# Performance work log

Hardware: AMD Instinct MI355X
Metric: run time of the kernel (lower is better)

Reference implementation:

```python
import jax, jax.numpy as jnp
import numpy as np

N = 50000      # nodes
M = 800000     # edges
D = 128        # node_state_dim == msg_dim
EF = 32        # edge_feat_dim
DF = 32        # node_dist_feat_dim
ATT = 128      # att_hidden_dim
L = 2          # num_layer (num_prop = 1)
IN = D + EF + DF  # 192, MLP input dim


def setup_inputs() -> dict:
    key = jax.random.key(0)
    ks = jax.random.split(key, 18)
    rn = lambda k, shape, s=0.05: jax.random.normal(k, shape, dtype=jnp.float32) * s
    return {
        "node_feat":   rn(ks[0], (N, D), 1.0),
        "node_feat_c": rn(ks[1], (N, D), 1.0),
        "edge":        jax.random.randint(ks[2], (M, 2), 0, N, dtype=jnp.int32),
        "edge_feat":   rn(ks[3], (M, EF), 1.0),
        "dist_feat":   rn(ks[4], (M, DF), 1.0),
        # msg MLP: Linear(IN->D) -> ReLU -> Linear(D->D), stacked over layers
        "msg_w0": rn(ks[5], (L, IN, D)),  "msg_b0": jnp.zeros((L, D), jnp.float32),
        "msg_w1": rn(ks[6], (L, D, D)),   "msg_b1": jnp.zeros((L, D), jnp.float32),
        # attention head: Linear(IN->ATT) -> ReLU -> Linear(ATT->D) -> Sigmoid
        "att_w0": rn(ks[7], (L, IN, ATT)), "att_b0": jnp.zeros((L, ATT), jnp.float32),
        "att_w1": rn(ks[8], (L, ATT, D)),  "att_b1": jnp.zeros((L, D), jnp.float32),
        # LSTMCell params (torch layout: W_ih [4H, in], W_hh [4H, H], gate order i,f,g,o)
        "lstm_wih": rn(ks[9],  (L, 4 * D, D)),
        "lstm_whh": rn(ks[10], (L, 4 * D, D)),
        "lstm_bih": jnp.zeros((L, 4 * D), jnp.float32),
        "lstm_bhh": jnp.zeros((L, 4 * D), jnp.float32),
    }


def _lstm_cell(x, h, c, wih, whh, bih, bhh):
    gates = x @ wih.T + bih + h @ whh.T + bhh          # [N, 4D]
    i, f, g, o = jnp.split(gates, 4, axis=1)
    c2 = jax.nn.sigmoid(f) * c + jax.nn.sigmoid(i) * jnp.tanh(g)
    h2 = jax.nn.sigmoid(o) * jnp.tanh(c2)
    return h2, c2


def reference(node_feat, node_feat_c, edge, edge_feat, dist_feat,
              msg_w0, msg_b0, msg_w1, msg_b1,
              att_w0, att_b0, att_w1, att_b1,
              lstm_wih, lstm_whh, lstm_bih, lstm_bhh):
    src = edge[:, 0]
    dst = edge[:, 1]
    state, state_c = node_feat, node_feat_c
    for ii in range(L):
        if ii > 0:
            state = jax.nn.relu(state)
        # _prop (num_prop = 1)
        state_diff = state[src] - state[dst]                               # [M, D]
        edge_input = jnp.concatenate([state_diff, edge_feat, dist_feat], 1)  # [M, IN]
        msg = jax.nn.relu(edge_input @ msg_w0[ii] + msg_b0[ii]) @ msg_w1[ii] + msg_b1[ii]
        att = jax.nn.sigmoid(
            jax.nn.relu(edge_input @ att_w0[ii] + att_b0[ii]) @ att_w1[ii] + att_b1[ii])
        msg = msg * att
        state_msg = jax.ops.segment_sum(msg, dst, num_segments=N)          # scatter_add
        state, state_c = _lstm_cell(state_msg, state, state_c,
                                    lstm_wih[ii], lstm_whh[ii],
                                    lstm_bih[ii], lstm_bhh[ii])
    return state
```

## Files before the change

kernel.cpp:

```cpp
#include <hip/hip_runtime.h>

constexpr int N  = 50000;
constexpr int M  = 800000;
constexpr int D  = 128;
constexpr int IN = 192;
constexpr int TE = 64;

typedef __attribute__((ext_vector_type(4)))  short short4v;
typedef __attribute__((ext_vector_type(8)))  short short8;
typedef __attribute__((ext_vector_type(16))) float f32x16;

__device__ __align__(16) short g_wp[163840];
__device__ __align__(16) short g_lw[262144];
__device__ __align__(16) short g_efdf[(size_t)M * 64];
__device__ __align__(16) short g_sbf[(size_t)N * D];
__device__ int g_cnt[N];
__device__ int g_ssrc[M];
__device__ int g_sdst[M];
__device__ int g_pos[M];

__device__ __forceinline__ float sigm(float x) { return 1.0f / (1.0f + __expf(-x)); }

__device__ __forceinline__ short f2bf(float f) {
    unsigned u = __builtin_bit_cast(unsigned, f);
    u = (u + 0x7FFFu + ((u >> 16) & 1u)) >> 16;
    return (short)u;
}
__device__ __forceinline__ float bf2f(short s) {
    return __builtin_bit_cast(float, ((unsigned)(unsigned short)s) << 16);
}

__global__ void zero_cnt_kernel() {
    for (int i = blockIdx.x * 256 + threadIdx.x; i < N; i += gridDim.x * 256) g_cnt[i] = 0;
}
__global__ void hist_kernel(const int* __restrict__ edge) {
    int e = blockIdx.x * 256 + threadIdx.x;
    if (e < M) atomicAdd(&g_cnt[edge[e * 2 + 1]], 1);
}
__global__ void scan_kernel() {
    __shared__ int partial[256];
    const int t = threadIdx.x;
    const int CH = (N + 255) / 256;
    const int base = t * CH;
    int sum = 0;
    for (int i = 0; i < CH; ++i) { int idx = base + i; if (idx < N) sum += g_cnt[idx]; }
    partial[t] = sum;
    __syncthreads();
    if (t == 0) { int acc = 0; for (int i = 0; i < 256; ++i) { int x = partial[i]; partial[i] = acc; acc += x; } }
    __syncthreads();
    int run = partial[t];
    for (int i = 0; i < CH; ++i) {
        int idx = base + i;
        if (idx < N) { int c = g_cnt[idx]; g_cnt[idx] = run; run += c; }
    }
}
__global__ void scatter_kernel(const int* __restrict__ edge) {
    int e = blockIdx.x * 256 + threadIdx.x;
    if (e < M) {
        const int s = edge[e * 2], d = edge[e * 2 + 1];
        const int p = atomicAdd(&g_cnt[d], 1);
        g_pos[e]  = p;
        g_ssrc[p] = s;
        g_sdst[p] = d;
    }
}

__global__ void pack_edge(const float* __restrict__ w0m, const float* __restrict__ w0a,
                          const float* __restrict__ w1m, const float* __restrict__ w1a) {
    int gid = blockIdx.x * 256 + threadIdx.x;
    int ii = gid / 81920;
    int r  = gid % 81920;
    int p  = r / 40960;  r %= 40960;
    int which = (r >= 24576) ? 1 : 0;
    int r2 = which ? r - 24576 : r;
    int e    = r2 & 7;
    int f    = r2 >> 3;
    int lane = f & 63;
    int ktct = f >> 6;
    int ct = ktct & 3, kt = ktct >> 2;
    int k   = kt * 16 + ((lane >> 5) << 3) + e;
    int col = ct * 32 + (lane & 31);
    const float* w0 = p ? w0a : w0m;
    const float* w1 = p ? w1a : w1m;
    float v = which ? w1[((size_t)ii * D + k) * D + col]
                    : w0[((size_t)ii * IN + k) * D + col];
    g_wp[gid] = f2bf(v);
}

__global__ void pack_lstm(const float* __restrict__ wih, const float* __restrict__ whh) {
    int gid = blockIdx.x * 256 + threadIdx.x;
    int ii = gid >> 17;
    int r  = gid & 131071;
    int e = r & 7, f = r >> 3;
    int lane = f & 63, rest = f >> 6;
    int cf = rest & 15, kt = rest >> 4;
    int col = cf * 32 + (lane & 31);
    int k   = (kt & 7) * 16 + ((lane >> 5) << 3) + e;
    const float* src = (kt < 8) ? wih : whh;
    g_lw[gid] = f2bf(src[((size_t)ii * 512 + col) * D + k]);
}

__global__ void pack_efdf(const float* __restrict__ ef, const float* __restrict__ df) {
    int gid = blockIdx.x * 256 + threadIdx.x;
    int e = gid >> 3, c0 = (gid & 7) * 8;
    const float* s = (c0 < 32) ? (ef + (size_t)e * 32 + c0) : (df + (size_t)e * 32 + (c0 - 32));
    float4 u0 = *(const float4*)s, u1 = *(const float4*)(s + 4);
    short8 t;
    t[0] = f2bf(u0.x); t[1] = f2bf(u0.y); t[2] = f2bf(u0.z); t[3] = f2bf(u0.w);
    t[4] = f2bf(u1.x); t[5] = f2bf(u1.y); t[6] = f2bf(u1.z); t[7] = f2bf(u1.w);
    const size_t pos = (size_t)g_pos[e];
    *(short8*)(g_efdf + pos * 64 + (size_t)(gid & 7) * 8) = t;
}

__global__ void init_kernel(const float4* __restrict__ nf, const float4* __restrict__ nfc,
                            float4* __restrict__ state, float4* __restrict__ state_c) {
    const int total = N * D / 4;
    for (int i = blockIdx.x * blockDim.x + threadIdx.x; i < total; i += gridDim.x * blockDim.x) {
        state[i]   = nf[i];
        state_c[i] = nfc[i];
    }
}

__global__ void prep_kernel(float4* __restrict__ state, float4* __restrict__ msg, int do_relu) {
    const int total = N * D / 4;
    const float4 z = make_float4(0.f, 0.f, 0.f, 0.f);
    for (int i = blockIdx.x * blockDim.x + threadIdx.x; i < total; i += gridDim.x * blockDim.x) {
        float4 v = state[i];
        if (do_relu) {
            v.x = fmaxf(v.x, 0.f); v.y = fmaxf(v.y, 0.f);
            v.z = fmaxf(v.z, 0.f); v.w = fmaxf(v.w, 0.f);
            state[i] = v;
        }
        short4v b;
        b[0] = f2bf(v.x); b[1] = f2bf(v.y); b[2] = f2bf(v.z); b[3] = f2bf(v.w);
        *(short4v*)(g_sbf + (size_t)i * 4) = b;
        msg[i] = z;
    }
}

__device__ __forceinline__ void stage_ld(const short8* __restrict__ gsrc, int gc, short8 g[4], int tid) {
    const short8* p = gsrc + (size_t)gc * 1024;
#pragma unroll
    for (int i = 0; i < 4; ++i) g[i] = p[tid + i * 256];
}
__device__ __forceinline__ void stage_st(short8* wb, int gc, const short8 g[4], int tid) {
    short8* d = wb + (gc & 1) * 1024;
#pragma unroll
    for (int i = 0; i < 4; ++i) d[tid + i * 256] = g[i];
}

template<int BASE>
__device__ __forceinline__ void gemm12(const short8* __restrict__ gsrc, short8* wb,
                                       const short8 a1[12], int tid, int lane, int cg,
                                       f32x16& o0, f32x16& o1) {
    f32x16 acc0 = {}, acc1 = {};
#pragma unroll
    for (int c = 0; c < 3; ++c) {
        const int gc = BASE + c;
        short8 g[4];
        if (gc + 1 < 10) stage_ld(gsrc, gc + 1, g, tid);
        const short8* buf = wb + (gc & 1) * 1024;
#pragma unroll
        for (int kl = 0; kl < 4; ++kl) {
            short8 b0 = buf[(kl * 4 + cg * 2 + 0) * 64 + lane];
            short8 b1 = buf[(kl * 4 + cg * 2 + 1) * 64 + lane];
            acc0 = __builtin_amdgcn_mfma_f32_32x32x16_bf16(a1[c * 4 + kl], b0, acc0, 0, 0, 0);
            acc1 = __builtin_amdgcn_mfma_f32_32x32x16_bf16(a1[c * 4 + kl], b1, acc1, 0, 0, 0);
        }
        if (gc + 1 < 10) stage_st(wb, gc + 1, g, tid);
        __syncthreads();
    }
    o0 = acc0; o1 = acc1;
}

template<int BASE>
__device__ __forceinline__ void gemm8(const short8* __restrict__ gsrc, short8* wb,
                                      const short (*hsr)[136], int tid, int lane, int cg, int half,
                                      f32x16& o0, f32x16& o1) {
    f32x16 acc0 = {}, acc1 = {};
#pragma unroll
    for (int c = 0; c < 2; ++c) {
        const int gc = BASE + c;
        short8 g[4];
        if (gc + 1 < 10) stage_ld(gsrc, gc + 1, g, tid);
        const short8* buf = wb + (gc & 1) * 1024;
#pragma unroll
        for (int kl = 0; kl < 4; ++kl) {
            const int kt = c * 4 + kl;
            short8 a2 = *(const short8*)&hsr[lane & 31][kt * 16 + half];
            short8 b0 = buf[(kl * 4 + cg * 2 + 0) * 64 + lane];
            short8 b1 = buf[(kl * 4 + cg * 2 + 1) * 64 + lane];
            acc0 = __builtin_amdgcn_mfma_f32_32x32x16_bf16(a2, b0, acc0, 0, 0, 0);
            acc1 = __builtin_amdgcn_mfma_f32_32x32x16_bf16(a2, b1, acc1, 0, 0, 0);
        }
        if (gc + 1 < 10) stage_st(wb, gc + 1, g, tid);
        __syncthreads();
    }
    o0 = acc0; o1 = acc1;
}

__device__ __forceinline__ void hwrite(short (*hsr)[136], const f32x16& a0, const f32x16& a1v,
                                       const float* __restrict__ b0, int lane, int cg) {
#pragma unroll
    for (int ct = 0; ct < 2; ++ct) {
        const int col = cg * 64 + ct * 32 + (lane & 31);
        const float bv = b0[col];
        f32x16 a = ct ? a1v : a0;
#pragma unroll
        for (int reg = 0; reg < 16; ++reg) {
            const int row = (reg & 3) + 8 * (reg >> 2) + 4 * (lane >> 5);
            hsr[row][col] = f2bf(fmaxf(a[reg] + bv, 0.f));
        }
    }
}

__global__ __launch_bounds__(256, 3)
void edge_mfma(int ii,
               const float* __restrict__ b0m, const float* __restrict__ b1m,
               const float* __restrict__ b0a, const float* __restrict__ b1a,
               float* __restrict__ state_msg) {
    __shared__ short8 wb[2048];
    __shared__ short  hs[2][32][136];
    __shared__ int    sdst[TE];

    const int tid  = threadIdx.x;
    const int lane = tid & 63;
    const int w    = tid >> 6;
    const int rt   = w >> 1, cg = w & 1;
    const int e0   = blockIdx.x * TE;

    if (tid < TE) sdst[tid] = g_sdst[e0 + tid];

    const int er   = e0 + rt * 32 + (lane & 31);
    const int half = (lane >> 5) << 3;
    const int s  = g_ssrc[er];
    const int d2 = g_sdst[er];
    const short* srow = g_sbf + (size_t)s  * D;
    const short* drow = g_sbf + (size_t)d2 * D;
    short8 a1[12];
#pragma unroll
    for (int kt = 0; kt < 8; ++kt) {
        const int k0 = kt * 16 + half;
        short8 sv = *(const short8*)(srow + k0);
        short8 dv = *(const short8*)(drow + k0);
        short8 t;
#pragma unroll
        for (int e = 0; e < 8; ++e) t[e] = f2bf(bf2f(sv[e]) - bf2f(dv[e]));
        a1[kt] = t;
    }
#pragma unroll
    for (int kt = 8; kt < 12; ++kt)
        a1[kt] = *(const short8*)(g_efdf + (size_t)er * 64 + (kt - 8) * 16 + half);

    const short8* gsrc = (const short8*)(g_wp + (size_t)ii * 81920);

    {
        short8 g[4];
        stage_ld(gsrc, 0, g, tid);
        stage_st(wb, 0, g, tid);
        __syncthreads();
    }

    f32x16 t0, t1, m0, m1, c0, c1;
    gemm12<0>(gsrc, (short8*)wb, a1, tid, lane, cg, t0, t1);
    hwrite(hs[rt], t0, t1, b0m, lane, cg);
    __syncthreads();
    gemm8<3>(gsrc, (short8*)wb, hs[rt], tid, lane, cg, half, m0, m1);
    gemm12<5>(gsrc, (short8*)wb, a1, tid, lane, cg, t0, t1);
    hwrite(hs[rt], t0, t1, b0a, lane, cg);
    __syncthreads();
    gemm8<8>(gsrc, (short8*)wb, hs[rt], tid, lane, cg, half, c0, c1);

    float (*vt)[D] = (float(*)[D])wb;
#pragma unroll
    for (int ct = 0; ct < 2; ++ct) {
        const int col = cg * 64 + ct * 32 + (lane & 31);
        const float bm = b1m[col], ba = b1a[col];
        f32x16 mv = ct ? m1 : m0;
        f32x16 av = ct ? c1 : c0;
#pragma unroll
        for (int reg = 0; reg < 16; ++reg) {
            const int row = rt * 32 + (reg & 3) + 8 * (reg >> 2) + 4 * (lane >> 5);
            vt[row][col] = (mv[reg] + bm) * sigm(av[reg] + ba);
        }
    }
    __syncthreads();

    const int colr = tid & 127;
    const int rbase = (tid >> 7) * 32;
    float run = 0.f;
    int cur = sdst[rbase];
#pragma unroll 4
    for (int r = 0; r < 32; ++r) {
        const int dd = sdst[rbase + r];
        if (dd != cur) {
            atomicAdd(state_msg + (size_t)cur * D + colr, run);
            run = 0.f; cur = dd;
        }
        run += vt[rbase + r][colr];
    }
    atomicAdd(state_msg + (size_t)cur * D + colr, run);
}

__global__ __launch_bounds__(256, 4)
void lstm_mfma(const float* __restrict__ x, float* __restrict__ hbuf, float* __restrict__ cbuf,
               int ii,
               const float* __restrict__ bih, const float* __restrict__ bhh) {
    __shared__ short8 wb[2048];
    const int tid  = threadIdx.x;
    const int lane = tid & 63;
    const int w    = tid >> 6;
    const int n0   = blockIdx.x * 32;
    const int half = (lane >> 5) << 3;
    const int nl   = lane & 31;
    const int nld  = min(n0 + nl, N - 1);

    const short8* gsrc = (const short8*)(g_lw + (size_t)ii * 131072);

    {
        short8 g[4];
#pragma unroll
        for (int i = 0; i < 4; ++i) g[i] = gsrc[tid + i * 256];
#pragma unroll
        for (int i = 0; i < 4; ++i) wb[tid + i * 256] = g[i];
        __syncthreads();
    }

    f32x16 acc[4] = {};
#pragma unroll
    for (int kt = 0; kt < 16; ++kt) {
        const float* srow = (kt < 8) ? (x + (size_t)nld * D + kt * 16 + half)
                                     : (hbuf + (size_t)nld * D + (kt - 8) * 16 + half);
        float4 u0 = *(const float4*)(srow);
        float4 u1 = *(const float4*)(srow + 4);
        short8 a;
        a[0] = f2bf(u0.x); a[1] = f2bf(u0.y); a[2] = f2bf(u0.z); a[3] = f2bf(u0.w);
        a[4] = f2bf(u1.x); a[5] = f2bf(u1.y); a[6] = f2bf(u1.z); a[7] = f2bf(u1.w);

        short8 g[4];
        if (kt + 1 < 16) {
            const short8* p = gsrc + (size_t)(kt + 1) * 1024;
#pragma unroll
            for (int i = 0; i < 4; ++i) g[i] = p[tid + i * 256];
        }
        const short8* buf = wb + (kt & 1) * 1024;
#pragma unroll
        for (int q = 0; q < 4; ++q) {
            short8 b = buf[(q * 4 + w) * 64 + lane];
            acc[q] = __builtin_amdgcn_mfma_f32_32x32x16_bf16(a, b, acc[q], 0, 0, 0);
        }
        if (kt + 1 < 16) {
            short8* d = wb + ((kt + 1) & 1) * 1024;
#pragma unroll
            for (int i = 0; i < 4; ++i) d[tid + i * 256] = g[i];
        }
        __syncthreads();
    }

    const int col = (w << 5) + nl;
    const float bi = bih[col]       + bhh[col];
    const float bf = bih[128 + col] + bhh[128 + col];
    const float bg = bih[256 + col] + bhh[256 + col];
    const float bo = bih[384 + col] + bhh[384 + col];
#pragma unroll
    for (int reg = 0; reg < 16; ++reg) {
        const int nn = (reg & 3) + 8 * (reg >> 2) + 4 * (lane >> 5);
        const int n = n0 + nn;
        if (n < N) {
            const float gi = acc[0][reg] + bi;
            const float gf = acc[1][reg] + bf;
            const float gg = acc[2][reg] + bg;
            const float go = acc[3][reg] + bo;
            float* cp = cbuf + (size_t)n * D + col;
            const float c2 = sigm(gf) * (*cp) + sigm(gi) * tanhf(gg);
            const float h2 = sigm(go) * tanhf(c2);
            *cp = c2;
            hbuf[(size_t)n * D + col] = h2;
        }
    }
}

extern "C" void kernel_launch(void* const* d_in, const int* in_sizes, int n_in,
                              void* d_out, int out_size, void* d_ws, size_t ws_size,
                              hipStream_t stream) {
    const float* node_feat   = (const float*)d_in[0];
    const float* node_feat_c = (const float*)d_in[1];
    const int*   edge        = (const int*)d_in[2];
    const float* edge_feat   = (const float*)d_in[3];
    const float* dist_feat   = (const float*)d_in[4];
    const float* msg_w0 = (const float*)d_in[5];
    const float* msg_b0 = (const float*)d_in[6];
    const float* msg_w1 = (const float*)d_in[7];
    const float* msg_b1 = (const float*)d_in[8];
    const float* att_w0 = (const float*)d_in[9];
    const float* att_b0 = (const float*)d_in[10];
    const float* att_w1 = (const float*)d_in[11];
    const float* att_b1 = (const float*)d_in[12];
    const float* lstm_wih = (const float*)d_in[13];
    const float* lstm_whh = (const float*)d_in[14];
    const float* lstm_bih = (const float*)d_in[15];
    const float* lstm_bhh = (const float*)d_in[16];

    float* state     = (float*)d_out;
    float* state_c   = (float*)d_ws;
    float* state_msg = (float*)d_ws + (size_t)N * D;

    zero_cnt_kernel<<<256, 256, 0, stream>>>();
    hist_kernel<<<(M + 255) / 256, 256, 0, stream>>>(edge);
    scan_kernel<<<1, 256, 0, stream>>>();
    scatter_kernel<<<(M + 255) / 256, 256, 0, stream>>>(edge);

    pack_efdf<<<25000, 256, 0, stream>>>(edge_feat, dist_feat);
    pack_edge<<<640, 256, 0, stream>>>(msg_w0, att_w0, msg_w1, att_w1);
    pack_lstm<<<1024, 256, 0, stream>>>(lstm_wih, lstm_whh);

    init_kernel<<<2048, 256, 0, stream>>>((const float4*)node_feat, (const float4*)node_feat_c,
                                          (float4*)state, (float4*)state_c);

    for (int ii = 0; ii < 2; ++ii) {
        prep_kernel<<<2048, 256, 0, stream>>>((float4*)state, (float4*)state_msg, ii > 0 ? 1 : 0);

        edge_mfma<<<M / TE, 256, 0, stream>>>(
            ii,
            msg_b0 + (size_t)ii * D, msg_b1 + (size_t)ii * D,
            att_b0 + (size_t)ii * D, att_b1 + (size_t)ii * D,
            state_msg);

        lstm_mfma<<<(N + 31) / 32, 256, 0, stream>>>(
            state_msg, state, state_c, ii,
            lstm_bih + (size_t)ii * 4 * D, lstm_bhh + (size_t)ii * 4 * D);
    }
}
```

Before: 967.7 us.

## Parallelize CSR scan, invert efdf packing, halve weight staging chunks for occupancy

Replaces the single-block prefix scan with a three-kernel multi-block scan. pack_efdf now gathers through an inverse permutation so its writes are coalesced. The edge kernel stages weights in half-size chunks (20 instead of 10), which shrinks the shared-memory pool so launch bounds can target 4 blocks per CU instead of 3. Float-to-bf16 conversions switch to packed paired intrinsics. The smaller chunks add more barriers per tile in exchange for higher occupancy.

```diff
diff --git a/kernel.cpp b/kernel.cpp
--- a/kernel.cpp
+++ b/kernel.cpp
@@ -1,10 +1,13 @@
 #include <hip/hip_runtime.h>
+#include <hip/hip_bf16.h>
 
 constexpr int N  = 50000;
 constexpr int M  = 800000;
 constexpr int D  = 128;
 constexpr int IN = 192;
 constexpr int TE = 64;
+constexpr int NCH = 20;
+constexpr int NBLK = (N + 255) / 256;
 
 typedef __attribute__((ext_vector_type(4)))  short short4v;
 typedef __attribute__((ext_vector_type(8)))  short short8;
@@ -15,9 +18,10 @@
 __device__ __align__(16) short g_efdf[(size_t)M * 64];
 __device__ __align__(16) short g_sbf[(size_t)N * D];
 __device__ int g_cnt[N];
+__device__ int g_part[NBLK];
 __device__ int g_ssrc[M];
 __device__ int g_sdst[M];
-__device__ int g_pos[M];
+__device__ int g_inv[M];
 
 __device__ __forceinline__ float sigm(float x) { return 1.0f / (1.0f + __expf(-x)); }
 
@@ -29,6 +33,12 @@
 __device__ __forceinline__ float bf2f(short s) {
     return __builtin_bit_cast(float, ((unsigned)(unsigned short)s) << 16);
 }
+__device__ __forceinline__ unsigned pk2(float a, float b) {
+    __hip_bfloat162 h = __float22bfloat162_rn(float2{a, b});
+    unsigned u;
+    __builtin_memcpy(&u, &h, 4);
+    return u;
+}
 
 __global__ void zero_cnt_kernel() {
     for (int i = blockIdx.x * 256 + threadIdx.x; i < N; i += gridDim.x * 256) g_cnt[i] = 0;
@@ -37,31 +47,58 @@
     int e = blockIdx.x * 256 + threadIdx.x;
     if (e < M) atomicAdd(&g_cnt[edge[e * 2 + 1]], 1);
 }
-__global__ void scan_kernel() {
-    __shared__ int partial[256];
+__global__ void scanA_kernel() {
+    __shared__ int red[256];
     const int t = threadIdx.x;
-    const int CH = (N + 255) / 256;
-    const int base = t * CH;
-    int sum = 0;
-    for (int i = 0; i < CH; ++i) { int idx = base + i; if (idx < N) sum += g_cnt[idx]; }
-    partial[t] = sum;
-    __syncthreads();
-    if (t == 0) { int acc = 0; for (int i = 0; i < 256; ++i) { int x = partial[i]; partial[i] = acc; acc += x; } }
-    __syncthreads();
-    int run = partial[t];
-    for (int i = 0; i < CH; ++i) {
-        int idx = base + i;
-        if (idx < N) { int c = g_cnt[idx]; g_cnt[idx] = run; run += c; }
-    }
+    const int idx = blockIdx.x * 256 + t;
+    red[t] = (idx < N) ? g_cnt[idx] : 0;
+    __syncthreads();
+#pragma unroll
+    for (int s = 128; s > 0; s >>= 1) {
+        if (t < s) red[t] += red[t + s];
+        __syncthreads();
+    }
+    if (t == 0) g_part[blockIdx.x] = red[0];
+}
+__global__ void scanB_kernel() {
+    __shared__ int sh[256];
+    const int t = threadIdx.x;
+    int v = (t < NBLK) ? g_part[t] : 0;
+    sh[t] = v;
+    __syncthreads();
+    int x = v;
+    for (int s = 1; s < 256; s <<= 1) {
+        int y = (t >= s) ? sh[t - s] : 0;
+        __syncthreads();
+        x += y; sh[t] = x;
+        __syncthreads();
+    }
+    if (t < NBLK) g_part[t] = x - v;
+}
+__global__ void scanC_kernel() {
+    __shared__ int sh[256];
+    const int t = threadIdx.x;
+    const int idx = blockIdx.x * 256 + t;
+    int v = (idx < N) ? g_cnt[idx] : 0;
+    sh[t] = v;
+    __syncthreads();
+    int x = v;
+    for (int s = 1; s < 256; s <<= 1) {
+        int y = (t >= s) ? sh[t - s] : 0;
+        __syncthreads();
+        x += y; sh[t] = x;
+        __syncthreads();
+    }
+    if (idx < N) g_cnt[idx] = g_part[blockIdx.x] + x - v;
 }
 __global__ void scatter_kernel(const int* __restrict__ edge) {
     int e = blockIdx.x * 256 + threadIdx.x;
     if (e < M) {
         const int s = edge[e * 2], d = edge[e * 2 + 1];
         const int p = atomicAdd(&g_cnt[d], 1);
-        g_pos[e]  = p;
         g_ssrc[p] = s;
         g_sdst[p] = d;
+        g_inv[p]  = e;
     }
 }
 
@@ -102,14 +139,15 @@
 
 __global__ void pack_efdf(const float* __restrict__ ef, const float* __restrict__ df) {
     int gid = blockIdx.x * 256 + threadIdx.x;
-    int e = gid >> 3, c0 = (gid & 7) * 8;
+    int p = gid >> 3, c0 = (gid & 7) * 8;
+    const int e = g_inv[p];
     const float* s = (c0 < 32) ? (ef + (size_t)e * 32 + c0) : (df + (size_t)e * 32 + (c0 - 32));
     float4 u0 = *(const float4*)s, u1 = *(const float4*)(s + 4);
     short8 t;
-    t[0] = f2bf(u0.x); t[1] = f2bf(u0.y); t[2] = f2bf(u0.z); t[3] = f2bf(u0.w);
-    t[4] = f2bf(u1.x); t[5] = f2bf(u1.y); t[6] = f2bf(u1.z); t[7] = f2bf(u1.w);
-    const size_t pos = (size_t)g_pos[e];
-    *(short8*)(g_efdf + pos * 64 + (size_t)(gid & 7) * 8) = t;
+    unsigned* tp = (unsigned*)&t;
+    tp[0] = pk2(u0.x, u0.y); tp[1] = pk2(u0.z, u0.w);
+    tp[2] = pk2(u1.x, u1.y); tp[3] = pk2(u1.z, u1.w);
+    *(short8*)(g_efdf + (size_t)gid * 8) = t;
 }
 
 __global__ void init_kernel(const float4* __restrict__ nf, const float4* __restrict__ nfc,
@@ -132,68 +170,69 @@
             state[i] = v;
         }
         short4v b;
-        b[0] = f2bf(v.x); b[1] = f2bf(v.y); b[2] = f2bf(v.z); b[3] = f2bf(v.w);
+        unsigned* bp = (unsigned*)&b;
+        bp[0] = pk2(v.x, v.y); bp[1] = pk2(v.z, v.w);
         *(short4v*)(g_sbf + (size_t)i * 4) = b;
         msg[i] = z;
     }
 }
 
-__device__ __forceinline__ void stage_ld(const short8* __restrict__ gsrc, int gc, short8 g[4], int tid) {
-    const short8* p = gsrc + (size_t)gc * 1024;
-#pragma unroll
-    for (int i = 0; i < 4; ++i) g[i] = p[tid + i * 256];
-}
-__device__ __forceinline__ void stage_st(short8* wb, int gc, const short8 g[4], int tid) {
-    short8* d = wb + (gc & 1) * 1024;
-#pragma unroll
-    for (int i = 0; i < 4; ++i) d[tid + i * 256] = g[i];
-}
+__device__ __forceinline__ void stage_ld(const short8* __restrict__ gsrc, int gc, short8 g[2], int tid) {
+    const short8* p = gsrc + (size_t)gc * 512;
+    g[0] = p[tid]; g[1] = p[tid + 256];
+}
+__device__ __forceinline__ void stage_st(short8* wb, int gc, const short8 g[2], int tid) {
+    short8* d = wb + (gc & 1) * 512;
+    d[tid] = g[0]; d[tid + 256] = g[1];
+}
+
+#define MFMA(a, b, c) __builtin_amdgcn_mfma_f32_32x32x16_bf16(a, b, c, 0, 0, 0)
 
 template<int BASE>
-__device__ __forceinline__ void gemm12(const short8* __restrict__ gsrc, short8* wb,
-                                       const short8 a1[12], int tid, int lane, int cg,
-                                       f32x16& o0, f32x16& o1) {
+__device__ __forceinline__ void gemmA(const short8* __restrict__ gsrc, short8* wb,
+                                      const short8 a1[12], int tid, int lane, int cg,
+                                      f32x16& o0, f32x16& o1) {
     f32x16 acc0 = {}, acc1 = {};
 #pragma unroll
-    for (int c = 0; c < 3; ++c) {
+    for (int c = 0; c < 6; ++c) {
         const int gc = BASE + c;
-        short8 g[4];
-        if (gc + 1 < 10) stage_ld(gsrc, gc + 1, g, tid);
-        const short8* buf = wb + (gc & 1) * 1024;
-#pragma unroll
-        for (int kl = 0; kl < 4; ++kl) {
+        short8 g[2];
+        if (gc + 1 < NCH) stage_ld(gsrc, gc + 1, g, tid);
+        const short8* buf = wb + (gc & 1) * 512;
+#pragma unroll
+        for (int kl = 0; kl < 2; ++kl) {
             short8 b0 = buf[(kl * 4 + cg * 2 + 0) * 64 + lane];
             short8 b1 = buf[(kl * 4 + cg * 2 + 1) * 64 + lane];
-            acc0 = __builtin_amdgcn_mfma_f32_32x32x16_bf16(a1[c * 4 + kl], b0, acc0, 0, 0, 0);
-            acc1 = __builtin_amdgcn_mfma_f32_32x32x16_bf16(a1[c * 4 + kl], b1, acc1, 0, 0, 0);
-        }
-        if (gc + 1 < 10) stage_st(wb, gc + 1, g, tid);
+            acc0 = MFMA(a1[c * 2 + kl], b0, acc0);
+            acc1 = MFMA(a1[c * 2 + kl], b1, acc1);
+        }
+        if (gc + 1 < NCH) stage_st(wb, gc + 1, g, tid);
         __syncthreads();
     }
     o0 = acc0; o1 = acc1;
 }
 
 template<int BASE>
-__device__ __forceinline__ void gemm8(const short8* __restrict__ gsrc, short8* wb,
+__device__ __forceinline__ void gemmH(const short8* __restrict__ gsrc, short8* wb,
                                       const short (*hsr)[136], int tid, int lane, int cg, int half,
                                       f32x16& o0, f32x16& o1) {
     f32x16 acc0 = {}, acc1 = {};
 #pragma unroll
-    for (int c = 0; c < 2; ++c) {
+    for (int c = 0; c < 4; ++c) {
         const int gc = BASE + c;
-        short8 g[4];
-        if (gc + 1 < 10) stage_ld(gsrc, gc + 1, g, tid);
-        const short8* buf = wb + (gc & 1) * 1024;
-#pragma unroll
-        for (int kl = 0; kl < 4; ++kl) {
-            const int kt = c * 4 + kl;
+        short8 g[2];
+        if (gc + 1 < NCH) stage_ld(gsrc, gc + 1, g, tid);
+        const short8* buf = wb + (gc & 1) * 512;
+#pragma unroll
+        for (int kl = 0; kl < 2; ++kl) {
+            const int kt = c * 2 + kl;
             short8 a2 = *(const short8*)&hsr[lane & 31][kt * 16 + half];
             short8 b0 = buf[(kl * 4 + cg * 2 + 0) * 64 + lane];
             short8 b1 = buf[(kl * 4 + cg * 2 + 1) * 64 + lane];
-            acc0 = __builtin_amdgcn_mfma_f32_32x32x16_bf16(a2, b0, acc0, 0, 0, 0);
-            acc1 = __builtin_amdgcn_mfma_f32_32x32x16_bf16(a2, b1, acc1, 0, 0, 0);
-        }
-        if (gc + 1 < 10) stage_st(wb, gc + 1, g, tid);
+            acc0 = MFMA(a2, b0, acc0);
+            acc1 = MFMA(a2, b1, acc1);
+        }
+        if (gc + 1 < NCH) stage_st(wb, gc + 1, g, tid);
         __syncthreads();
     }
     o0 = acc0; o1 = acc1;
@@ -207,21 +246,25 @@
         const float bv = b0[col];
         f32x16 a = ct ? a1v : a0;
 #pragma unroll
-        for (int reg = 0; reg < 16; ++reg) {
+        for (int rp = 0; rp < 8; ++rp) {
+            const int reg = rp * 2;
             const int row = (reg & 3) + 8 * (reg >> 2) + 4 * (lane >> 5);
-            hsr[row][col] = f2bf(fmaxf(a[reg] + bv, 0.f));
-        }
-    }
-}
-
-__global__ __launch_bounds__(256, 3)
+            const unsigned pr = pk2(fmaxf(a[reg] + bv, 0.f), fmaxf(a[reg + 1] + bv, 0.f));
+            hsr[row][col]     = (short)(pr & 0xFFFF);
+            hsr[row + 1][col] = (short)(pr >> 16);
+        }
+    }
+}
+
+__global__ __launch_bounds__(256, 4)
 void edge_mfma(int ii,
                const float* __restrict__ b0m, const float* __restrict__ b1m,
                const float* __restrict__ b0a, const float* __restrict__ b1a,
                float* __restrict__ state_msg) {
-    __shared__ short8 wb[2048];
-    __shared__ short  hs[2][32][136];
-    __shared__ int    sdst[TE];
+    __shared__ __align__(16) char pool[34048];
+    short8* wb = (short8*)pool;
+    short (*hs)[32][136] = (short(*)[32][136])(pool + 16384);
+    int* sdst = (int*)(pool + 33792);
 
     const int tid  = threadIdx.x;
     const int lane = tid & 63;
@@ -244,8 +287,11 @@
         short8 sv = *(const short8*)(srow + k0);
         short8 dv = *(const short8*)(drow + k0);
         short8 t;
-#pragma unroll
-        for (int e = 0; e < 8; ++e) t[e] = f2bf(bf2f(sv[e]) - bf2f(dv[e]));
+        unsigned* tp = (unsigned*)&t;
+#pragma unroll
+        for (int i = 0; i < 4; ++i)
+            tp[i] = pk2(bf2f(sv[2 * i])     - bf2f(dv[2 * i]),
+                        bf2f(sv[2 * i + 1]) - bf2f(dv[2 * i + 1]));
         a1[kt] = t;
     }
 #pragma unroll
@@ -255,23 +301,23 @@
     const short8* gsrc = (const short8*)(g_wp + (size_t)ii * 81920);
 
     {
-        short8 g[4];
+        short8 g[2];
         stage_ld(gsrc, 0, g, tid);
         stage_st(wb, 0, g, tid);
         __syncthreads();
     }
 
     f32x16 t0, t1, m0, m1, c0, c1;
-    gemm12<0>(gsrc, (short8*)wb, a1, tid, lane, cg, t0, t1);
+    gemmA<0>(gsrc, wb, a1, tid, lane, cg, t0, t1);
     hwrite(hs[rt], t0, t1, b0m, lane, cg);
     __syncthreads();
-    gemm8<3>(gsrc, (short8*)wb, hs[rt], tid, lane, cg, half, m0, m1);
-    gemm12<5>(gsrc, (short8*)wb, a1, tid, lane, cg, t0, t1);
+    gemmH<6>(gsrc, wb, hs[rt], tid, lane, cg, half, m0, m1);
+    gemmA<10>(gsrc, wb, a1, tid, lane, cg, t0, t1);
     hwrite(hs[rt], t0, t1, b0a, lane, cg);
     __syncthreads();
-    gemm8<8>(gsrc, (short8*)wb, hs[rt], tid, lane, cg, half, c0, c1);
-
-    float (*vt)[D] = (float(*)[D])wb;
+    gemmH<16>(gsrc, wb, hs[rt], tid, lane, cg, half, c0, c1);
+
+    float (*vt)[D] = (float(*)[D])pool;
 #pragma unroll
     for (int ct = 0; ct < 2; ++ct) {
         const int col = cg * 64 + ct * 32 + (lane & 31);
@@ -334,8 +380,9 @@
         float4 u0 = *(const float4*)(srow);
         float4 u1 = *(const float4*)(srow + 4);
         short8 a;
-        a[0] = f2bf(u0.x); a[1] = f2bf(u0.y); a[2] = f2bf(u0.z); a[3] = f2bf(u0.w);
-        a[4] = f2bf(u1.x); a[5] = f2bf(u1.y); a[6] = f2bf(u1.z); a[7] = f2bf(u1.w);
+        unsigned* ap = (unsigned*)&a;
+        ap[0] = pk2(u0.x, u0.y); ap[1] = pk2(u0.z, u0.w);
+        ap[2] = pk2(u1.x, u1.y); ap[3] = pk2(u1.z, u1.w);
 
         short8 g[4];
         if (kt + 1 < 16) {
@@ -347,7 +394,7 @@
 #pragma unroll
         for (int q = 0; q < 4; ++q) {
             short8 b = buf[(q * 4 + w) * 64 + lane];
-            acc[q] = __builtin_amdgcn_mfma_f32_32x32x16_bf16(a, b, acc[q], 0, 0, 0);
+            acc[q] = MFMA(a, b, acc[q]);
         }
         if (kt + 1 < 16) {
             short8* d = wb + ((kt + 1) & 1) * 1024;
@@ -407,7 +454,9 @@
 
     zero_cnt_kernel<<<256, 256, 0, stream>>>();
     hist_kernel<<<(M + 255) / 256, 256, 0, stream>>>(edge);
-    scan_kernel<<<1, 256, 0, stream>>>();
+    scanA_kernel<<<NBLK, 256, 0, stream>>>();
+    scanB_kernel<<<1, 256, 0, stream>>>();
+    scanC_kernel<<<NBLK, 256, 0, stream>>>();
     scatter_kernel<<<(M + 255) / 256, 256, 0, stream>>>(edge);
 
     pack_efdf<<<25000, 256, 0, stream>>>(edge_feat, dist_feat);
```

Measured after the change: 931.4 us. 3.7% less time.
